# Optimization experiments

Measured on AMD Instinct MI355X. Metric: run time of the kernel, lower is better.

The kernel has to match this reference:

```python
import jax, jax.numpy as jnp
import numpy as np


def setup_inputs() -> dict:
    key = jax.random.key(0)
    k1, k2 = jax.random.split(key)
    # (C, N, 2) projected circle points; only circle 0 is used
    img_render_points = jax.random.normal(k1, (2, 4096, 2), dtype=jnp.float32) * 100.0
    # (K, M, 2) skeleton slices; only the last slice is used
    ref_catheter_skeleton = jax.random.normal(k2, (2, 32768, 2), dtype=jnp.float32) * 100.0
    return {"img_render_points": img_render_points,
            "ref_catheter_skeleton": ref_catheter_skeleton}


def reference(img_render_points, ref_catheter_skeleton):
    # first projected circle -> (N, 2)
    pts = img_render_points[0].reshape(-1, 2)
    # last skeleton slice, point order flipped (flip is math-neutral for chamfer) -> (M, 2)
    ref = ref_catheter_skeleton[-1][::-1]
    # pairwise Euclidean distances (N, M) via the squared-norm expansion
    # ||a-b||^2 = ||a||^2 + ||b||^2 - 2 a.b  (avoids materializing (N, M, 2))
    sq = (jnp.sum(pts * pts, axis=1)[:, None]
          + jnp.sum(ref * ref, axis=1)[None, :]
          - 2.0 * (pts @ ref.T))
    dist = jnp.sqrt(jnp.maximum(sq, 1e-12))  # (N, M)
    chamfer = jnp.sum(jnp.min(dist, axis=1)) + jnp.sum(jnp.min(dist, axis=0))
    return chamfer
```

## Files before the change

### kernel.cpp

```cpp
#include <hip/hip_runtime.h>


typedef float v2f __attribute__((ext_vector_type(2)));

constexpr int N_PTS = 4096;
constexpr int M_REF = 32768;

__device__ __forceinline__ v2f pk_fma(v2f a, v2f b, v2f c) {
    v2f d;
    asm("v_pk_fma_f32 %0, %1, %2, %3" : "=v"(d) : "v"(a), "v"(b), "v"(c));
    return d;
}
__device__ __forceinline__ v2f pk_mul(v2f a, v2f b) {
    v2f d;
    asm("v_pk_mul_f32 %0, %1, %2" : "=v"(d) : "v"(a), "v"(b));
    return d;
}

__global__ __launch_bounds__(512) void chamfer_fused(
    const float2* __restrict__ pts, const float2* __restrict__ refs,
    float* __restrict__ partial)
{
    __shared__ float redA[128];
    __shared__ float redB[24];
    const int tid = threadIdx.x, b = blockIdx.x;
    const int lane = tid & 63, wave = tid >> 6;
    const float4* pts4  = (const float4*)pts;
    const float4* refs4 = (const float4*)refs;

    v2f px2[16], py2[16];
    float mn[16];
    #pragma unroll
    for (int q = 0; q < 8; ++q) {
        const float4 o = pts4[b * 8 + q];
        px2[2*q]   = (v2f){-2.f*o.x, -2.f*o.x};
        py2[2*q]   = (v2f){-2.f*o.y, -2.f*o.y};
        px2[2*q+1] = (v2f){-2.f*o.z, -2.f*o.z};
        py2[2*q+1] = (v2f){-2.f*o.w, -2.f*o.w};
    }
    #pragma unroll
    for (int k = 0; k < 16; ++k) mn[k] = 3.0e38f;

    #pragma unroll 4
    for (int i = 0; i < 32; ++i) {
        const float4 rr = refs4[tid + 512 * i];
        const v2f rx2 = (v2f){rr.x, rr.z};
        const v2f ry2 = (v2f){rr.y, rr.w};
        const v2f rz2 = pk_fma(rx2, rx2, pk_mul(ry2, ry2));
        #pragma unroll
        for (int k = 0; k < 16; ++k) {
            const v2f d2 = pk_fma(px2[k], rx2, pk_fma(py2[k], ry2, rz2));
            mn[k] = fminf(fminf(mn[k], d2.x), d2.y);
        }
    }
    #pragma unroll
    for (int k = 0; k < 16; ++k) {
        #pragma unroll
        for (int m = 1; m < 64; m <<= 1)
            mn[k] = fminf(mn[k], __shfl_xor(mn[k], m, 64));
    }
    if (lane == 0) {
        #pragma unroll
        for (int k = 0; k < 16; ++k) redA[wave * 16 + k] = mn[k];
    }
    __syncthreads();
    if (tid < 16) {
        float m = redA[tid];
        #pragma unroll
        for (int w = 1; w < 8; ++w) m = fminf(m, redA[w * 16 + tid]);
        const float2 p = pts[b * 16 + tid];
        redB[tid] = sqrtf(fmaxf(m + fmaf(p.x, p.x, p.y * p.y), 1e-12f));
    }

    v2f rxs[16], rys[16];
    float n2r[16];
    #pragma unroll
    for (int q = 0; q < 8; ++q) {
        const float4 o = refs4[b * 64 + wave * 8 + q];
        rxs[2*q]   = (v2f){-2.f*o.x, -2.f*o.x};
        rys[2*q]   = (v2f){-2.f*o.y, -2.f*o.y};
        n2r[2*q]   = fmaf(o.x, o.x, o.y * o.y);
        rxs[2*q+1] = (v2f){-2.f*o.z, -2.f*o.z};
        rys[2*q+1] = (v2f){-2.f*o.w, -2.f*o.w};
        n2r[2*q+1] = fmaf(o.z, o.z, o.w * o.w);
    }
    #pragma unroll
    for (int k = 0; k < 16; ++k) mn[k] = 3.0e38f;

    #pragma unroll 4
    for (int i = 0; i < 32; ++i) {
        const float4 pp = pts4[lane + 64 * i];
        const v2f pxx = (v2f){pp.x, pp.z};
        const v2f pyy = (v2f){pp.y, pp.w};
        const v2f pzz = pk_fma(pxx, pxx, pk_mul(pyy, pyy));
        #pragma unroll
        for (int k = 0; k < 16; ++k) {
            const v2f d2 = pk_fma(rxs[k], pxx, pk_fma(rys[k], pyy, pzz));
            mn[k] = fminf(fminf(mn[k], d2.x), d2.y);
        }
    }
    #pragma unroll
    for (int k = 0; k < 16; ++k) {
        #pragma unroll
        for (int m = 1; m < 64; m <<= 1)
            mn[k] = fminf(mn[k], __shfl_xor(mn[k], m, 64));
    }
    if (lane == 0) {
        float s = 0.f;
        #pragma unroll
        for (int k = 0; k < 16; ++k)
            s += sqrtf(fmaxf(mn[k] + n2r[k], 1e-12f));
        redB[16 + wave] = s;
    }
    __syncthreads();
    if (tid == 0) {
        float t = 0.f;
        #pragma unroll
        for (int k = 0; k < 24; ++k) t += redB[k];
        partial[b] = t;
    }
}

__global__ __launch_bounds__(256) void chamfer_sum(
    const float* __restrict__ partial, float* __restrict__ out)
{
    __shared__ float ssum[4];
    const int tid = threadIdx.x;
    float d = partial[tid];
    #pragma unroll
    for (int off = 32; off > 0; off >>= 1) d += __shfl_down(d, off, 64);
    const int lane = tid & 63, wave = tid >> 6;
    if (lane == 0) ssum[wave] = d;
    __syncthreads();
    if (tid == 0) out[0] = ssum[0] + ssum[1] + ssum[2] + ssum[3];
}

extern "C" void kernel_launch(void* const* d_in, const int* in_sizes, int n_in,
                              void* d_out, int out_size, void* d_ws, size_t ws_size,
                              hipStream_t stream) {
    const float2* pts  = (const float2*)d_in[0];
    const float2* refs = ((const float2*)d_in[1]) + M_REF;

    float* partial = (float*)d_ws;
    float* out = (float*)d_out;

    chamfer_fused<<<256, 512, 0, stream>>>(pts, refs, partial);
    chamfer_sum  <<<1, 256, 0, stream>>>(partial, out);
}
```

Baseline: 32.00 us.

## Interleave both chamfer directions in one loop and double grid to 512 blocks

Each block now owns 8 query points and 8 ref points per wave instead of 16, and the grid doubles to 512 blocks. The two direction passes (points→refs and refs→points) are merged into a single loop so both loads and both min-updates interleave, and one mid-kernel barrier is removed. The aim is more blocks across CUs and better latency hiding, at the cost of smaller per-thread reuse and twice as many partials to reduce.

```diff
diff --git a/kernel.cpp b/kernel.cpp
--- a/kernel.cpp
+++ b/kernel.cpp
@@ -17,114 +17,106 @@
     return d;
 }
 
-__global__ __launch_bounds__(512) void chamfer_fused(
+__global__ __launch_bounds__(512, 4) void chamfer_fused(
     const float2* __restrict__ pts, const float2* __restrict__ refs,
     float* __restrict__ partial)
 {
-    __shared__ float redA[128];
-    __shared__ float redB[24];
+    __shared__ float redA[64];
+    __shared__ float redB[16];
     const int tid = threadIdx.x, b = blockIdx.x;
     const int lane = tid & 63, wave = tid >> 6;
     const float4* pts4  = (const float4*)pts;
     const float4* refs4 = (const float4*)refs;
 
-    v2f px2[16], py2[16];
-    float mn[16];
+    v2f pxA[8], pyA[8]; float mnA[8];
     #pragma unroll
-    for (int q = 0; q < 8; ++q) {
-        const float4 o = pts4[b * 8 + q];
-        px2[2*q]   = (v2f){-2.f*o.x, -2.f*o.x};
-        py2[2*q]   = (v2f){-2.f*o.y, -2.f*o.y};
-        px2[2*q+1] = (v2f){-2.f*o.z, -2.f*o.z};
-        py2[2*q+1] = (v2f){-2.f*o.w, -2.f*o.w};
+    for (int q = 0; q < 4; ++q) {
+        const float4 o = pts4[b * 4 + q];
+        pxA[2*q]   = (v2f){-2.f*o.x, -2.f*o.x};
+        pyA[2*q]   = (v2f){-2.f*o.y, -2.f*o.y};
+        pxA[2*q+1] = (v2f){-2.f*o.z, -2.f*o.z};
+        pyA[2*q+1] = (v2f){-2.f*o.w, -2.f*o.w};
+    }
+    v2f rxB[8], ryB[8]; float n2B[8], mnB[8];
+    #pragma unroll
+    for (int q = 0; q < 4; ++q) {
+        const float4 o = refs4[b * 32 + wave * 4 + q];
+        rxB[2*q]   = (v2f){-2.f*o.x, -2.f*o.x};
+        ryB[2*q]   = (v2f){-2.f*o.y, -2.f*o.y};
+        n2B[2*q]   = fmaf(o.x, o.x, o.y * o.y);
+        rxB[2*q+1] = (v2f){-2.f*o.z, -2.f*o.z};
+        ryB[2*q+1] = (v2f){-2.f*o.w, -2.f*o.w};
+        n2B[2*q+1] = fmaf(o.z, o.z, o.w * o.w);
     }
     #pragma unroll
-    for (int k = 0; k < 16; ++k) mn[k] = 3.0e38f;
+    for (int k = 0; k < 8; ++k) { mnA[k] = 3.0e38f; mnB[k] = 3.0e38f; }
 
-    #pragma unroll 4
+    #pragma unroll 2
     for (int i = 0; i < 32; ++i) {
-        const float4 rr = refs4[tid + 512 * i];
+        const float4 rr = refs4[tid  + 512 * i];
+        const float4 pp = pts4 [lane +  64 * i];
         const v2f rx2 = (v2f){rr.x, rr.z};
         const v2f ry2 = (v2f){rr.y, rr.w};
         const v2f rz2 = pk_fma(rx2, rx2, pk_mul(ry2, ry2));
         #pragma unroll
-        for (int k = 0; k < 16; ++k) {
-            const v2f d2 = pk_fma(px2[k], rx2, pk_fma(py2[k], ry2, rz2));
-            mn[k] = fminf(fminf(mn[k], d2.x), d2.y);
+        for (int k = 0; k < 8; ++k) {
+            const v2f d2 = pk_fma(pxA[k], rx2, pk_fma(pyA[k], ry2, rz2));
+            mnA[k] = fminf(fminf(mnA[k], d2.x), d2.y);
+        }
+        const v2f px2 = (v2f){pp.x, pp.z};
+        const v2f py2 = (v2f){pp.y, pp.w};
+        const v2f pz2 = pk_fma(px2, px2, pk_mul(py2, py2));
+        #pragma unroll
+        for (int k = 0; k < 8; ++k) {
+            const v2f d2 = pk_fma(rxB[k], px2, pk_fma(ryB[k], py2, pz2));
+            mnB[k] = fminf(fminf(mnB[k], d2.x), d2.y);
         }
     }
+
     #pragma unroll
-    for (int k = 0; k < 16; ++k) {
+    for (int k = 0; k < 8; ++k) {
         #pragma unroll
         for (int m = 1; m < 64; m <<= 1)
-            mn[k] = fminf(mn[k], __shfl_xor(mn[k], m, 64));
+            mnA[k] = fminf(mnA[k], __shfl_xor(mnA[k], m, 64));
     }
     if (lane == 0) {
         #pragma unroll
-        for (int k = 0; k < 16; ++k) redA[wave * 16 + k] = mn[k];
-    }
-    __syncthreads();
-    if (tid < 16) {
-        float m = redA[tid];
-        #pragma unroll
-        for (int w = 1; w < 8; ++w) m = fminf(m, redA[w * 16 + tid]);
-        const float2 p = pts[b * 16 + tid];
-        redB[tid] = sqrtf(fmaxf(m + fmaf(p.x, p.x, p.y * p.y), 1e-12f));
-    }
-
-    v2f rxs[16], rys[16];
-    float n2r[16];
-    #pragma unroll
-    for (int q = 0; q < 8; ++q) {
-        const float4 o = refs4[b * 64 + wave * 8 + q];
-        rxs[2*q]   = (v2f){-2.f*o.x, -2.f*o.x};
-        rys[2*q]   = (v2f){-2.f*o.y, -2.f*o.y};
-        n2r[2*q]   = fmaf(o.x, o.x, o.y * o.y);
-        rxs[2*q+1] = (v2f){-2.f*o.z, -2.f*o.z};
-        rys[2*q+1] = (v2f){-2.f*o.w, -2.f*o.w};
-        n2r[2*q+1] = fmaf(o.z, o.z, o.w * o.w);
+        for (int k = 0; k < 8; ++k) redA[wave * 8 + k] = mnA[k];
     }
     #pragma unroll
-    for (int k = 0; k < 16; ++k) mn[k] = 3.0e38f;
-
-    #pragma unroll 4
-    for (int i = 0; i < 32; ++i) {
-        const float4 pp = pts4[lane + 64 * i];
-        const v2f pxx = (v2f){pp.x, pp.z};
-        const v2f pyy = (v2f){pp.y, pp.w};
-        const v2f pzz = pk_fma(pxx, pxx, pk_mul(pyy, pyy));
-        #pragma unroll
-        for (int k = 0; k < 16; ++k) {
-            const v2f d2 = pk_fma(rxs[k], pxx, pk_fma(rys[k], pyy, pzz));
-            mn[k] = fminf(fminf(mn[k], d2.x), d2.y);
-        }
-    }
-    #pragma unroll
-    for (int k = 0; k < 16; ++k) {
+    for (int k = 0; k < 8; ++k) {
         #pragma unroll
         for (int m = 1; m < 64; m <<= 1)
-            mn[k] = fminf(mn[k], __shfl_xor(mn[k], m, 64));
+            mnB[k] = fminf(mnB[k], __shfl_xor(mnB[k], m, 64));
     }
     if (lane == 0) {
         float s = 0.f;
         #pragma unroll
-        for (int k = 0; k < 16; ++k)
-            s += sqrtf(fmaxf(mn[k] + n2r[k], 1e-12f));
-        redB[16 + wave] = s;
+        for (int k = 0; k < 8; ++k)
+            s += sqrtf(fmaxf(mnB[k] + n2B[k], 1e-12f));
+        redB[8 + wave] = s;
+    }
+    __syncthreads();
+    if (tid < 8) {
+        float m = redA[tid];
+        #pragma unroll
+        for (int w = 1; w < 8; ++w) m = fminf(m, redA[w * 8 + tid]);
+        const float2 p = pts[b * 8 + tid];
+        redB[tid] = sqrtf(fmaxf(m + fmaf(p.x, p.x, p.y * p.y), 1e-12f));
     }
     __syncthreads();
     if (tid == 0) {
         float t = 0.f;
         #pragma unroll
-        for (int k = 0; k < 24; ++k) t += redB[k];
+        for (int k = 0; k < 16; ++k) t += redB[k];
         partial[b] = t;
     }
 }
 
-__global__ __launch_bounds__(256) void chamfer_sum(
+__global__ __launch_bounds__(512) void chamfer_sum(
     const float* __restrict__ partial, float* __restrict__ out)
 {
-    __shared__ float ssum[4];
+    __shared__ float ssum[8];
     const int tid = threadIdx.x;
     float d = partial[tid];
     #pragma unroll
@@ -132,7 +124,12 @@
     const int lane = tid & 63, wave = tid >> 6;
     if (lane == 0) ssum[wave] = d;
     __syncthreads();
-    if (tid == 0) out[0] = ssum[0] + ssum[1] + ssum[2] + ssum[3];
+    if (tid == 0) {
+        float t = 0.f;
+        #pragma unroll
+        for (int w = 0; w < 8; ++w) t += ssum[w];
+        out[0] = t;
+    }
 }
 
 extern "C" void kernel_launch(void* const* d_in, const int* in_sizes, int n_in,
@@ -144,6 +141,6 @@
     float* partial = (float*)d_ws;
     float* out = (float*)d_out;
 
-    chamfer_fused<<<256, 512, 0, stream>>>(pts, refs, partial);
-    chamfer_sum  <<<1, 256, 0, stream>>>(partial, out);
+    chamfer_fused<<<512, 512, 0, stream>>>(pts, refs, partial);
+    chamfer_sum  <<<1, 512, 0, stream>>>(partial, out);
 }
```

New measurement: 30.42 us. -4.9%, faster.

## Interleave both chamfer direction loops into one loop with batched loads

Applied to the files above, without the earlier changes.

Merges the two sequential min-distance loops (points→refs and refs→points) into one loop, so each iteration issues four ref loads and four point loads up front and then processes both directions. The aim is more independent work and memory parallelism per wave, and to remove the serial dependence between the two phases. It also recomputes the ref norms from the stored -2x values instead of keeping a separate array. In exchange it doubles the live register set (two coordinate and min arrays), which may reduce occupancy or cause spills.

```diff
diff --git a/kernel.cpp b/kernel.cpp
--- a/kernel.cpp
+++ b/kernel.cpp
@@ -28,40 +28,79 @@
     const float4* pts4  = (const float4*)pts;
     const float4* refs4 = (const float4*)refs;
 
-    v2f px2[16], py2[16];
-    float mn[16];
+    v2f pxA[16], pyA[16]; float mnA[16];
     #pragma unroll
     for (int q = 0; q < 8; ++q) {
         const float4 o = pts4[b * 8 + q];
-        px2[2*q]   = (v2f){-2.f*o.x, -2.f*o.x};
-        py2[2*q]   = (v2f){-2.f*o.y, -2.f*o.y};
-        px2[2*q+1] = (v2f){-2.f*o.z, -2.f*o.z};
-        py2[2*q+1] = (v2f){-2.f*o.w, -2.f*o.w};
+        pxA[2*q]   = (v2f){-2.f*o.x, -2.f*o.x};
+        pyA[2*q]   = (v2f){-2.f*o.y, -2.f*o.y};
+        pxA[2*q+1] = (v2f){-2.f*o.z, -2.f*o.z};
+        pyA[2*q+1] = (v2f){-2.f*o.w, -2.f*o.w};
+    }
+    v2f rxB[16], ryB[16]; float mnB[16];
+    #pragma unroll
+    for (int q = 0; q < 8; ++q) {
+        const float4 o = refs4[b * 64 + wave * 8 + q];
+        rxB[2*q]   = (v2f){-2.f*o.x, -2.f*o.x};
+        ryB[2*q]   = (v2f){-2.f*o.y, -2.f*o.y};
+        rxB[2*q+1] = (v2f){-2.f*o.z, -2.f*o.z};
+        ryB[2*q+1] = (v2f){-2.f*o.w, -2.f*o.w};
     }
     #pragma unroll
-    for (int k = 0; k < 16; ++k) mn[k] = 3.0e38f;
+    for (int k = 0; k < 16; ++k) { mnA[k] = 3.0e38f; mnB[k] = 3.0e38f; }
 
-    #pragma unroll 4
-    for (int i = 0; i < 32; ++i) {
-        const float4 rr = refs4[tid + 512 * i];
-        const v2f rx2 = (v2f){rr.x, rr.z};
-        const v2f ry2 = (v2f){rr.y, rr.w};
-        const v2f rz2 = pk_fma(rx2, rx2, pk_mul(ry2, ry2));
+    for (int o = 0; o < 8; ++o) {
+        float4 rr[4], pp[4];
         #pragma unroll
-        for (int k = 0; k < 16; ++k) {
-            const v2f d2 = pk_fma(px2[k], rx2, pk_fma(py2[k], ry2, rz2));
-            mn[k] = fminf(fminf(mn[k], d2.x), d2.y);
+        for (int u = 0; u < 4; ++u) {
+            rr[u] = refs4[tid  + 512 * (4 * o + u)];
+            pp[u] = pts4 [lane +  64 * (4 * o + u)];
         }
+        #pragma unroll
+        for (int u = 0; u < 4; ++u) {
+            const v2f rx2 = (v2f){rr[u].x, rr[u].z};
+            const v2f ry2 = (v2f){rr[u].y, rr[u].w};
+            const v2f rz2 = pk_fma(rx2, rx2, pk_mul(ry2, ry2));
+            #pragma unroll
+            for (int k = 0; k < 16; ++k) {
+                const v2f d2 = pk_fma(pxA[k], rx2, pk_fma(pyA[k], ry2, rz2));
+                mnA[k] = fminf(fminf(mnA[k], d2.x), d2.y);
+            }
+            const v2f px2 = (v2f){pp[u].x, pp[u].z};
+            const v2f py2 = (v2f){pp[u].y, pp[u].w};
+            const v2f pz2 = pk_fma(px2, px2, pk_mul(py2, py2));
+            #pragma unroll
+            for (int k = 0; k < 16; ++k) {
+                const v2f d2 = pk_fma(rxB[k], px2, pk_fma(ryB[k], py2, pz2));
+                mnB[k] = fminf(fminf(mnB[k], d2.x), d2.y);
+            }
+        }
+    }
+
+    #pragma unroll
+    for (int k = 0; k < 16; ++k) {
+        #pragma unroll
+        for (int m = 1; m < 64; m <<= 1)
+            mnA[k] = fminf(mnA[k], __shfl_xor(mnA[k], m, 64));
+    }
+    if (lane == 0) {
+        #pragma unroll
+        for (int k = 0; k < 16; ++k) redA[wave * 16 + k] = mnA[k];
     }
     #pragma unroll
     for (int k = 0; k < 16; ++k) {
         #pragma unroll
         for (int m = 1; m < 64; m <<= 1)
-            mn[k] = fminf(mn[k], __shfl_xor(mn[k], m, 64));
+            mnB[k] = fminf(mnB[k], __shfl_xor(mnB[k], m, 64));
     }
     if (lane == 0) {
+        float s = 0.f;
         #pragma unroll
-        for (int k = 0; k < 16; ++k) redA[wave * 16 + k] = mn[k];
+        for (int k = 0; k < 16; ++k) {
+            const float n2 = 0.25f * fmaf(rxB[k].x, rxB[k].x, ryB[k].x * ryB[k].x);
+            s += sqrtf(fmaxf(mnB[k] + n2, 1e-12f));
+        }
+        redB[16 + wave] = s;
     }
     __syncthreads();
     if (tid < 16) {
@@ -70,47 +109,6 @@
         for (int w = 1; w < 8; ++w) m = fminf(m, redA[w * 16 + tid]);
         const float2 p = pts[b * 16 + tid];
         redB[tid] = sqrtf(fmaxf(m + fmaf(p.x, p.x, p.y * p.y), 1e-12f));
-    }
-
-    v2f rxs[16], rys[16];
-    float n2r[16];
-    #pragma unroll
-    for (int q = 0; q < 8; ++q) {
-        const float4 o = refs4[b * 64 + wave * 8 + q];
-        rxs[2*q]   = (v2f){-2.f*o.x, -2.f*o.x};
-        rys[2*q]   = (v2f){-2.f*o.y, -2.f*o.y};
-        n2r[2*q]   = fmaf(o.x, o.x, o.y * o.y);
-        rxs[2*q+1] = (v2f){-2.f*o.z, -2.f*o.z};
-        rys[2*q+1] = (v2f){-2.f*o.w, -2.f*o.w};
-        n2r[2*q+1] = fmaf(o.z, o.z, o.w * o.w);
-    }
-    #pragma unroll
-    for (int k = 0; k < 16; ++k) mn[k] = 3.0e38f;
-
-    #pragma unroll 4
-    for (int i = 0; i < 32; ++i) {
-        const float4 pp = pts4[lane + 64 * i];
-        const v2f pxx = (v2f){pp.x, pp.z};
-        const v2f pyy = (v2f){pp.y, pp.w};
-        const v2f pzz = pk_fma(pxx, pxx, pk_mul(pyy, pyy));
-        #pragma unroll
-        for (int k = 0; k < 16; ++k) {
-            const v2f d2 = pk_fma(rxs[k], pxx, pk_fma(rys[k], pyy, pzz));
-            mn[k] = fminf(fminf(mn[k], d2.x), d2.y);
-        }
-    }
-    #pragma unroll
-    for (int k = 0; k < 16; ++k) {
-        #pragma unroll
-        for (int m = 1; m < 64; m <<= 1)
-            mn[k] = fminf(mn[k], __shfl_xor(mn[k], m, 64));
-    }
-    if (lane == 0) {
-        float s = 0.f;
-        #pragma unroll
-        for (int k = 0; k < 16; ++k)
-            s += sqrtf(fmaxf(mn[k] + n2r[k], 1e-12f));
-        redB[16 + wave] = s;
     }
     __syncthreads();
     if (tid == 0) {
```

Measured after the change: 29.51 us. 7.8% less time.
